# Performance work log

Measured on AMD Instinct MI355X. Metric: run time of the kernel, lower is better.

The kernel has to match this reference:

```python
import jax, jax.numpy as jnp
import numpy as np

B, C, H, W = 256, 768, 14, 14
S = 196  # sample_size
HID = 512
OUT = 2


def setup_inputs() -> dict:
    key = jax.random.key(0)
    ks = jax.random.split(key, 10)
    x = jax.random.normal(ks[0], (B, C, H, W), dtype=jnp.float32)
    pxs = jax.random.randint(ks[1], (B, S, 2), 0, H, dtype=jnp.int32)
    pys = jax.random.randint(ks[2], (B, S, 2), 0, H, dtype=jnp.int32)
    scale = 0.02
    W1 = jax.random.normal(ks[3], (2 * C, HID), dtype=jnp.float32) * scale
    b1 = jnp.zeros((HID,), dtype=jnp.float32)
    W2 = jax.random.normal(ks[4], (HID, HID), dtype=jnp.float32) * scale
    b2 = jnp.zeros((HID,), dtype=jnp.float32)
    W3 = jax.random.normal(ks[5], (HID, OUT), dtype=jnp.float32) * scale
    b3 = jnp.zeros((OUT,), dtype=jnp.float32)
    return {"x": x, "W1": W1, "b1": b1, "W2": W2, "b2": b2,
            "W3": W3, "b3": b3, "pxs": pxs, "pys": pys}


def _gather_pts(x_flat, pxy):
    # x_flat: [B, C, H*W]; pxy: [B, S, 2] -> [B, S, C]
    idx = pxy[:, :, 0] * W + pxy[:, :, 1]            # [B, S]
    g = jnp.take_along_axis(x_flat, idx[:, None, :].astype(jnp.int32), axis=2)  # [B, C, S]
    return g.transpose(0, 2, 1)                       # [B, S, C]


def reference(x, W1, b1, W2, b2, W3, b3, pxs, pys):
    x_flat = x.reshape(B, C, H * W)
    ptsx = _gather_pts(x_flat, pxs)                   # [B, S, C]
    ptsy = _gather_pts(x_flat, pys)                   # [B, S, C]
    feats = jnp.concatenate([ptsx, ptsy], axis=2)     # [B, S, 2C]
    h = jax.nn.relu(feats @ W1 + b1)
    h = jax.nn.relu(h @ W2 + b2)
    pred = h @ W3 + b3                                # [B, S, 2]
    predxy = pred.reshape(-1, OUT)                    # [B*S, 2]
    # use_abs=False, normalize=False: deltaxy = (pxs - pys) + (H - 1)
    deltaxy = (pxs - pys).astype(jnp.float32).reshape(-1, 2) + (H - 1)
    return predxy, deltaxy
```

## Files before the change

### kernel.cpp

```cpp
#include <hip/hip_runtime.h>
#include <hip/hip_bf16.h>

typedef __attribute__((ext_vector_type(4))) float f32x4;
typedef __attribute__((ext_vector_type(4))) int   int4v;
typedef __attribute__((ext_vector_type(8))) int   int8v;

__device__ __forceinline__ unsigned char f2fp8(float f) {
    unsigned char s = (__float_as_uint(f) >> 24) & 0x80;
    float a = fabsf(f);
    if (a >= 448.f) return s | 0x7E;
    if (a < 0.015625f) {
        int q = (int)(a * 512.0f + 0.5f);
        return s | (unsigned char)q;
    }
    unsigned int u = __float_as_uint(a);
    u += 0x0007FFFF + ((u >> 20) & 1);
    int e8 = (int)((u >> 23) & 0xFF) - 120;
    if (e8 >= 16) return s | 0x7E;
    return s | (unsigned char)((e8 << 3) | ((u >> 20) & 7));
}
__device__ __forceinline__ void gload_lds16(const void* g, void* l) {
    __builtin_amdgcn_global_load_lds((const __attribute__((address_space(1))) void*)g,
                                     (__attribute__((address_space(3))) void*)l, 16, 0, 0);
}

#define BATCH 256
#define CHAN  768
#define HW    196
#define SPS   196
#define HID   512
#define MROWS 50176
#define K1    1536
#define WSCL  64.0f
#define WINV  0.015625f
#define SC1   0x7F7F7F7F


__global__ void transpose_cast_fp8(const float* __restrict__ in, unsigned char* __restrict__ out,
                                   int K, int N) {
    int idx = blockIdx.x * 256 + threadIdx.x;
    if (idx >= K * N) return;
    int n = idx / K, k = idx - n * K;
    out[idx] = f2fp8(in[(size_t)k * N + n] * WSCL);
}

__global__ __launch_bounds__(256) void gather_feats(const float* __restrict__ x,
                                                    const int* __restrict__ pxs,
                                                    const int* __restrict__ pys,
                                                    unsigned char* __restrict__ feats,
                                                    float* __restrict__ out) {
    __shared__ float lds[64 * 197];
    int chunk = blockIdx.x;
    int b     = blockIdx.y;
    int c0 = chunk * 64;
    const float* xb = x + ((size_t)b * CHAN + c0) * HW;
    for (int t = threadIdx.x; t < 64 * HW; t += 256) {
        int j = t / HW, p = t - j * HW;
        lds[j * 197 + p] = xb[t];
    }
    if (chunk == 0) {
        for (int i = threadIdx.x; i < SPS * 2; i += 256) {
            int idx = b * SPS * 2 + i;
            out[MROWS * 2 + idx] = (float)(pxs[idx] - pys[idx]) + 13.0f;
        }
    }
    __syncthreads();
    int wid = threadIdx.x >> 6, lane = threadIdx.x & 63;
    int g = lane >> 4;
    int cq = (lane & 15) * 4;
    for (int sb = wid * 4; sb < SPS; sb += 16) {
        int s = sb + g;
        int base = (b * SPS + s) * 2;
        int ix = pxs[base] * 14 + pxs[base + 1];
        int iy = pys[base] * 14 + pys[base + 1];
        const float* lx = lds + cq * 197;
        unsigned int ux = 0, uy = 0;
        ux = __builtin_amdgcn_cvt_pk_fp8_f32(lx[ix],       lx[197 + ix], ux, false);
        ux = __builtin_amdgcn_cvt_pk_fp8_f32(lx[394 + ix], lx[591 + ix], ux, true);
        uy = __builtin_amdgcn_cvt_pk_fp8_f32(lx[iy],       lx[197 + iy], uy, false);
        uy = __builtin_amdgcn_cvt_pk_fp8_f32(lx[394 + iy], lx[591 + iy], uy, true);
        size_t ro = (size_t)(b * SPS + s) * K1;
        *(unsigned int*)(feats + ro + c0 + cq)        = ux;
        *(unsigned int*)(feats + ro + CHAN + c0 + cq) = uy;
    }
}

__global__ __launch_bounds__(512, 1) void mlp_fused(const unsigned char* __restrict__ feats,
                                                    const unsigned char* __restrict__ W1t,
                                                    const float* __restrict__ b1,
                                                    const unsigned char* __restrict__ W2t,
                                                    const float* __restrict__ b2,
                                                    const float* __restrict__ W3,
                                                    const float* __restrict__ b3,
                                                    float* __restrict__ out) {
    extern __shared__ char smem[];
    const int t = threadIdx.x;
    const int wid = t >> 6, lane = t & 63;
    const int wr = wid >> 2, wcn = wid & 3;
    const int lr = lane & 15, lk = lane >> 4;
    const int mBase = blockIdx.x * 128;
    f32x4 acc[4][8] = {};

    auto stage1 = [&](int buf, int kt) {
        char* Ab = smem + buf * 16384;
        char* Bb = smem + 32768 + buf * 65536;
        #pragma unroll
        for (int i = 0; i < 2; ++i) {
            int lin = i * 512 + t, row = lin >> 3, cs = (lin & 7) ^ (row & 7);
            gload_lds16(feats + (size_t)(mBase + row) * K1 + kt * 128 + cs * 16,
                        Ab + lin * 16);
        }
        #pragma unroll
        for (int i = 0; i < 8; ++i) {
            int lin = i * 512 + t, row = lin >> 3, cs = (lin & 7) ^ (row & 7);
            gload_lds16(W1t + (size_t)row * K1 + kt * 128 + cs * 16,
                        Bb + lin * 16);
        }
    };
    auto frag128 = [&](const char* rowp, int r) -> int8v {
        union { int4v h[2]; int8v v; } u;
        u.h[0] = *(const int4v*)(rowp + (((2 * lk + 0) ^ (r & 7)) * 16));
        u.h[1] = *(const int4v*)(rowp + (((2 * lk + 1) ^ (r & 7)) * 16));
        return u.v;
    };
    auto compute1 = [&](int buf) {
        const char* Ab = smem + buf * 16384;
        const char* Bb = smem + 32768 + buf * 65536;
        int8v af[4];
        #pragma unroll
        for (int m = 0; m < 4; ++m) {
            int r = wr * 64 + m * 16 + lr;
            af[m] = frag128(Ab + r * 128, r);
        }
        #pragma unroll
        for (int half = 0; half < 2; ++half) {
            int8v bf4[4];
            #pragma unroll
            for (int n = 0; n < 4; ++n) {
                int r = wcn * 128 + (half * 4 + n) * 16 + lr;
                bf4[n] = frag128(Bb + r * 128, r);
            }
            #pragma unroll
            for (int m = 0; m < 4; ++m)
                #pragma unroll
                for (int n = 0; n < 4; ++n)
                    acc[m][half * 4 + n] = __builtin_amdgcn_mfma_scale_f32_16x16x128_f8f6f4(
                        af[m], bf4[n], acc[m][half * 4 + n], 0, 0, 0, SC1, 0, SC1);
        }
    };

    stage1(0, 0);
    __syncthreads();
    int cur = 0;
    for (int kt = 0; kt < 12; ++kt) {
        if (kt + 1 < 12) stage1(cur ^ 1, kt + 1);
        compute1(cur);
        __syncthreads();
        cur ^= 1;
    }

    char* h1l = smem + 32768;
    char* B2b0 = smem;
    char* B2b1 = smem + 16384;
    #pragma unroll
    for (int n = 0; n < 8; ++n) {
        int c = wcn * 128 + n * 16 + lr;
        int c16 = wcn * 8 + n;
        float bv = b1[c];
        #pragma unroll
        for (int m = 0; m < 4; ++m) {
            int r0 = wr * 64 + m * 16 + lk * 4;
            float v0 = fmaxf(acc[m][n][0] * WINV + bv, 0.f);
            float v1 = fmaxf(acc[m][n][1] * WINV + bv, 0.f);
            float v2 = fmaxf(acc[m][n][2] * WINV + bv, 0.f);
            float v3 = fmaxf(acc[m][n][3] * WINV + bv, 0.f);
            unsigned int u = __builtin_amdgcn_cvt_pk_fp8_f32(v0, v1, 0u, false);
            u = __builtin_amdgcn_cvt_pk_fp8_f32(v2, v3, u, true);
            #pragma unroll
            for (int j = 0; j < 4; ++j) {
                int r = r0 + j;
                h1l[r * 512 + ((c16 ^ (r & 31)) * 16) + lr] =
                    (unsigned char)((u >> (8 * j)) & 0xff);
            }
        }
    }

    auto stageB2 = [&](char* dst, int p) {
        #pragma unroll
        for (int i = 0; i < 2; ++i) {
            int lin = i * 512 + t, row2 = lin >> 5, c = lin & 31;
            gload_lds16(W2t + (size_t)(p * 32 + row2) * 512 + ((c ^ row2) * 16),
                        dst + lin * 16);
        }
    };
    auto frag512 = [&](const char* base, int r, int kt2) -> int8v {
        int g = kt2 * 8 + lk * 2;
        union { int4v h[2]; int8v v; } u;
        u.h[0] = *(const int4v*)(base + r * 512 + (((g + 0) ^ (r & 31)) * 16));
        u.h[1] = *(const int4v*)(base + r * 512 + (((g + 1) ^ (r & 31)) * 16));
        return u.v;
    };

    float pp0[4] = {0.f, 0.f, 0.f, 0.f}, pp1[4] = {0.f, 0.f, 0.f, 0.f};
    stageB2(B2b0, 0);
    __syncthreads();
    for (int p = 0; p < 16; ++p) {
        char* curB = (p & 1) ? B2b1 : B2b0;
        char* nxtB = (p & 1) ? B2b0 : B2b1;
        if (p + 1 < 16) stageB2(nxtB, p + 1);
        f32x4 acc2[2] = {};
        #pragma unroll
        for (int kt2 = 0; kt2 < 4; ++kt2) {
            int8v a2 = frag512(h1l, wid * 16 + lr, kt2);
            #pragma unroll
            for (int n2 = 0; n2 < 2; ++n2) {
                int8v b2f = frag512(curB, n2 * 16 + lr, kt2);
                acc2[n2] = __builtin_amdgcn_mfma_scale_f32_16x16x128_f8f6f4(
                    a2, b2f, acc2[n2], 0, 0, 0, SC1, 0, SC1);
            }
        }
        #pragma unroll
        for (int n2 = 0; n2 < 2; ++n2) {
            int c2 = p * 32 + n2 * 16 + lr;
            float bv = b2[c2], w30 = W3[c2 * 2], w31 = W3[c2 * 2 + 1];
            #pragma unroll
            for (int j = 0; j < 4; ++j) {
                float v = fmaxf(acc2[n2][j] * WINV + bv, 0.f);
                pp0[j] += v * w30;
                pp1[j] += v * w31;
            }
        }
        __syncthreads();
    }

    float bb0 = b3[0], bb1 = b3[1];
    #pragma unroll
    for (int j = 0; j < 4; ++j) {
        float p0 = pp0[j], p1 = pp1[j];
        #pragma unroll
        for (int msk = 1; msk < 16; msk <<= 1) {
            p0 += __shfl_xor(p0, msk);
            p1 += __shfl_xor(p1, msk);
        }
        if (lr == 0) {
            int r = mBase + wid * 16 + lk * 4 + j;
            out[(size_t)r * 2 + 0] = p0 + bb0;
            out[(size_t)r * 2 + 1] = p1 + bb1;
        }
    }
}

extern "C" void kernel_launch(void* const* d_in, const int* in_sizes, int n_in,
                              void* d_out, int out_size, void* d_ws, size_t ws_size,
                              hipStream_t stream) {
    const float* x  = (const float*)d_in[0];
    const float* W1 = (const float*)d_in[1];
    const float* b1 = (const float*)d_in[2];
    const float* W2 = (const float*)d_in[3];
    const float* b2 = (const float*)d_in[4];
    const float* W3 = (const float*)d_in[5];
    const float* b3 = (const float*)d_in[6];
    const int*  pxs = (const int*)d_in[7];
    const int*  pys = (const int*)d_in[8];
    float* out = (float*)d_out;
    char* ws = (char*)d_ws;

    unsigned char* W1t   = (unsigned char*)(ws + 0);
    unsigned char* W2t   = (unsigned char*)(ws + 786432);
    unsigned char* feats = (unsigned char*)(ws + 1048576);

    hipFuncSetAttribute((const void*)mlp_fused,
                        hipFuncAttributeMaxDynamicSharedMemorySize, 163840);

    transpose_cast_fp8<<<(K1 * HID + 255) / 256, 256, 0, stream>>>(W1, W1t, K1, HID);
    transpose_cast_fp8<<<(HID * HID + 255) / 256, 256, 0, stream>>>(W2, W2t, HID, HID);
    gather_feats<<<dim3(12, BATCH), 256, 0, stream>>>(x, pxs, pys, feats, out);
    mlp_fused<<<MROWS / 128, 512, 163840, stream>>>(feats, W1t, b1, W2t, b2, W3, b3, out);
}
```

Measured before the change: 166.3 us.

## Double MLP block to 16 waves and keep W2 fragments in registers

The fused MLP kernel goes from 512 to 1024 threads per block. Each wave now owns a 64-column slice of layer 1 instead of 128, which halves the accumulator registers per thread. For layer 2, each wave loads its 32-column slice of W2 directly from global memory into registers and loops over all 128 rows of h1. This removes the double-buffered LDS staging of W2 and its per-step barriers. Partial layer-3 sums are then reduced across waves through an LDS buffer, which adds one barrier and a small reduction step, and register pressure per thread may limit how well the larger block schedules.

Result: slower. 271.0 us (+62.9%).

```diff
diff --git a/kernel.cpp b/kernel.cpp
--- a/kernel.cpp
+++ b/kernel.cpp
@@ -85,34 +85,33 @@
     }
 }
 
-__global__ __launch_bounds__(512, 1) void mlp_fused(const unsigned char* __restrict__ feats,
-                                                    const unsigned char* __restrict__ W1t,
-                                                    const float* __restrict__ b1,
-                                                    const unsigned char* __restrict__ W2t,
-                                                    const float* __restrict__ b2,
-                                                    const float* __restrict__ W3,
-                                                    const float* __restrict__ b3,
-                                                    float* __restrict__ out) {
+__global__ __launch_bounds__(1024) void mlp_fused(const unsigned char* __restrict__ feats,
+                                                  const unsigned char* __restrict__ W1t,
+                                                  const float* __restrict__ b1,
+                                                  const unsigned char* __restrict__ W2t,
+                                                  const float* __restrict__ b2,
+                                                  const float* __restrict__ W3,
+                                                  const float* __restrict__ b3,
+                                                  float* __restrict__ out) {
     extern __shared__ char smem[];
     const int t = threadIdx.x;
     const int wid = t >> 6, lane = t & 63;
-    const int wr = wid >> 2, wcn = wid & 3;
+    const int wr = wid >> 3, wcn = wid & 7;
     const int lr = lane & 15, lk = lane >> 4;
     const int mBase = blockIdx.x * 128;
-    f32x4 acc[4][8] = {};
+    f32x4 acc[4][4] = {};
 
     auto stage1 = [&](int buf, int kt) {
         char* Ab = smem + buf * 16384;
         char* Bb = smem + 32768 + buf * 65536;
-        #pragma unroll
-        for (int i = 0; i < 2; ++i) {
-            int lin = i * 512 + t, row = lin >> 3, cs = (lin & 7) ^ (row & 7);
+        {
+            int lin = t, row = lin >> 3, cs = (lin & 7) ^ (row & 7);
             gload_lds16(feats + (size_t)(mBase + row) * K1 + kt * 128 + cs * 16,
                         Ab + lin * 16);
         }
         #pragma unroll
-        for (int i = 0; i < 8; ++i) {
-            int lin = i * 512 + t, row = lin >> 3, cs = (lin & 7) ^ (row & 7);
+        for (int i = 0; i < 4; ++i) {
+            int lin = i * 1024 + t, row = lin >> 3, cs = (lin & 7) ^ (row & 7);
             gload_lds16(W1t + (size_t)row * K1 + kt * 128 + cs * 16,
                         Bb + lin * 16);
         }
@@ -133,19 +132,13 @@
             af[m] = frag128(Ab + r * 128, r);
         }
         #pragma unroll
-        for (int half = 0; half < 2; ++half) {
-            int8v bf4[4];
-            #pragma unroll
-            for (int n = 0; n < 4; ++n) {
-                int r = wcn * 128 + (half * 4 + n) * 16 + lr;
-                bf4[n] = frag128(Bb + r * 128, r);
-            }
+        for (int n = 0; n < 4; ++n) {
+            int r = wcn * 64 + n * 16 + lr;
+            int8v bf = frag128(Bb + r * 128, r);
             #pragma unroll
             for (int m = 0; m < 4; ++m)
-                #pragma unroll
-                for (int n = 0; n < 4; ++n)
-                    acc[m][half * 4 + n] = __builtin_amdgcn_mfma_scale_f32_16x16x128_f8f6f4(
-                        af[m], bf4[n], acc[m][half * 4 + n], 0, 0, 0, SC1, 0, SC1);
+                acc[m][n] = __builtin_amdgcn_mfma_scale_f32_16x16x128_f8f6f4(
+                    af[m], bf, acc[m][n], 0, 0, 0, SC1, 0, SC1);
         }
     };
 
@@ -159,13 +152,21 @@
         cur ^= 1;
     }
 
+    int8v b2f[2][4];
+    #pragma unroll
+    for (int n2 = 0; n2 < 2; ++n2) {
+        const unsigned char* rp = W2t + (size_t)(wid * 32 + n2 * 16 + lr) * 512;
+        #pragma unroll
+        for (int kt2 = 0; kt2 < 4; ++kt2)
+            b2f[n2][kt2] = *(const int8v*)(rp + kt2 * 128 + lk * 32);
+    }
+
     char* h1l = smem + 32768;
-    char* B2b0 = smem;
-    char* B2b1 = smem + 16384;
+    float* red = (float*)smem;
     #pragma unroll
-    for (int n = 0; n < 8; ++n) {
-        int c = wcn * 128 + n * 16 + lr;
-        int c16 = wcn * 8 + n;
+    for (int n = 0; n < 4; ++n) {
+        int c = wcn * 64 + n * 16 + lr;
+        int c16 = wcn * 4 + n;
         float bv = b1[c];
         #pragma unroll
         for (int m = 0; m < 4; ++m) {
@@ -184,69 +185,61 @@
             }
         }
     }
-
-    auto stageB2 = [&](char* dst, int p) {
-        #pragma unroll
-        for (int i = 0; i < 2; ++i) {
-            int lin = i * 512 + t, row2 = lin >> 5, c = lin & 31;
-            gload_lds16(W2t + (size_t)(p * 32 + row2) * 512 + ((c ^ row2) * 16),
-                        dst + lin * 16);
-        }
-    };
-    auto frag512 = [&](const char* base, int r, int kt2) -> int8v {
+    __syncthreads();
+
+    auto frag512 = [&](int r, int kt2) -> int8v {
         int g = kt2 * 8 + lk * 2;
         union { int4v h[2]; int8v v; } u;
-        u.h[0] = *(const int4v*)(base + r * 512 + (((g + 0) ^ (r & 31)) * 16));
-        u.h[1] = *(const int4v*)(base + r * 512 + (((g + 1) ^ (r & 31)) * 16));
+        u.h[0] = *(const int4v*)(h1l + r * 512 + (((g + 0) ^ (r & 31)) * 16));
+        u.h[1] = *(const int4v*)(h1l + r * 512 + (((g + 1) ^ (r & 31)) * 16));
         return u.v;
     };
-
-    float pp0[4] = {0.f, 0.f, 0.f, 0.f}, pp1[4] = {0.f, 0.f, 0.f, 0.f};
-    stageB2(B2b0, 0);
-    __syncthreads();
-    for (int p = 0; p < 16; ++p) {
-        char* curB = (p & 1) ? B2b1 : B2b0;
-        char* nxtB = (p & 1) ? B2b0 : B2b1;
-        if (p + 1 < 16) stageB2(nxtB, p + 1);
+    #pragma unroll
+    for (int s = 0; s < 8; ++s) {
         f32x4 acc2[2] = {};
         #pragma unroll
         for (int kt2 = 0; kt2 < 4; ++kt2) {
-            int8v a2 = frag512(h1l, wid * 16 + lr, kt2);
-            #pragma unroll
-            for (int n2 = 0; n2 < 2; ++n2) {
-                int8v b2f = frag512(curB, n2 * 16 + lr, kt2);
-                acc2[n2] = __builtin_amdgcn_mfma_scale_f32_16x16x128_f8f6f4(
-                    a2, b2f, acc2[n2], 0, 0, 0, SC1, 0, SC1);
-            }
-        }
+            int8v a2 = frag512(s * 16 + lr, kt2);
+            acc2[0] = __builtin_amdgcn_mfma_scale_f32_16x16x128_f8f6f4(
+                a2, b2f[0][kt2], acc2[0], 0, 0, 0, SC1, 0, SC1);
+            acc2[1] = __builtin_amdgcn_mfma_scale_f32_16x16x128_f8f6f4(
+                a2, b2f[1][kt2], acc2[1], 0, 0, 0, SC1, 0, SC1);
+        }
+        float p0[4] = {0.f, 0.f, 0.f, 0.f}, p1[4] = {0.f, 0.f, 0.f, 0.f};
         #pragma unroll
         for (int n2 = 0; n2 < 2; ++n2) {
-            int c2 = p * 32 + n2 * 16 + lr;
+            int c2 = wid * 32 + n2 * 16 + lr;
             float bv = b2[c2], w30 = W3[c2 * 2], w31 = W3[c2 * 2 + 1];
             #pragma unroll
             for (int j = 0; j < 4; ++j) {
                 float v = fmaxf(acc2[n2][j] * WINV + bv, 0.f);
-                pp0[j] += v * w30;
-                pp1[j] += v * w31;
-            }
-        }
-        __syncthreads();
-    }
-
-    float bb0 = b3[0], bb1 = b3[1];
-    #pragma unroll
-    for (int j = 0; j < 4; ++j) {
-        float p0 = pp0[j], p1 = pp1[j];
-        #pragma unroll
-        for (int msk = 1; msk < 16; msk <<= 1) {
-            p0 += __shfl_xor(p0, msk);
-            p1 += __shfl_xor(p1, msk);
-        }
-        if (lr == 0) {
-            int r = mBase + wid * 16 + lk * 4 + j;
-            out[(size_t)r * 2 + 0] = p0 + bb0;
-            out[(size_t)r * 2 + 1] = p1 + bb1;
-        }
+                p0[j] += v * w30;
+                p1[j] += v * w31;
+            }
+        }
+        #pragma unroll
+        for (int j = 0; j < 4; ++j) {
+            #pragma unroll
+            for (int msk = 1; msk < 16; msk <<= 1) {
+                p0[j] += __shfl_xor(p0[j], msk);
+                p1[j] += __shfl_xor(p1[j], msk);
+            }
+            if (lr == 0) {
+                int r = s * 16 + lk * 4 + j;
+                red[r * 33 + wid * 2 + 0] = p0[j];
+                red[r * 33 + wid * 2 + 1] = p1[j];
+            }
+        }
+    }
+    __syncthreads();
+
+    if (t < 256) {
+        int row = t >> 1, comp = t & 1;
+        float v = b3[comp];
+        #pragma unroll
+        for (int w = 0; w < 16; ++w)
+            v += red[row * 33 + w * 2 + comp];
+        out[(size_t)(mBase + row) * 2 + comp] = v;
     }
 }
 
@@ -275,5 +268,5 @@
     transpose_cast_fp8<<<(K1 * HID + 255) / 256, 256, 0, stream>>>(W1, W1t, K1, HID);
     transpose_cast_fp8<<<(HID * HID + 255) / 256, 256, 0, stream>>>(W2, W2t, HID, HID);
     gather_feats<<<dim3(12, BATCH), 256, 0, stream>>>(x, pxs, pys, feats, out);
-    mlp_fused<<<MROWS / 128, 512, 163840, stream>>>(feats, W1t, b1, W2t, b2, W3, b3, out);
-}
+    mlp_fused<<<MROWS / 128, 1024, 163840, stream>>>(feats, W1t, b1, W2t, b2, W3, b3, out);
+}
```

## Keep W2 fragments in registers and split layer-2 columns across waves

Applied to the files above, without the earlier changes.

Layer 2 used to stream W2 through LDS in 16 double-buffered passes, each wave handling 16 rows against every column. Now each wave loads its own 64 output columns of W2 directly into registers once and loops over all 128 rows of h1 from LDS. Per-wave partial sums for layer 3 are combined through a small LDS reduction buffer. This removes 16 barrier-synchronised staging steps, at the cost of a large register footprint (64 int registers for the B fragments) and an extra cross-wave reduction.

Measured after the change: 192.6 us. 15.8% more time.

```diff
diff --git a/kernel.cpp b/kernel.cpp
--- a/kernel.cpp
+++ b/kernel.cpp
@@ -160,8 +160,7 @@
     }
 
     char* h1l = smem + 32768;
-    char* B2b0 = smem;
-    char* B2b1 = smem + 16384;
+    float* red = (float*)smem;
     #pragma unroll
     for (int n = 0; n < 8; ++n) {
         int c = wcn * 128 + n * 16 + lr;
@@ -184,69 +183,76 @@
             }
         }
     }
-
-    auto stageB2 = [&](char* dst, int p) {
-        #pragma unroll
-        for (int i = 0; i < 2; ++i) {
-            int lin = i * 512 + t, row2 = lin >> 5, c = lin & 31;
-            gload_lds16(W2t + (size_t)(p * 32 + row2) * 512 + ((c ^ row2) * 16),
-                        dst + lin * 16);
-        }
-    };
-    auto frag512 = [&](const char* base, int r, int kt2) -> int8v {
+    __syncthreads();
+
+    int8v b2f[4][4];
+    #pragma unroll
+    for (int n2 = 0; n2 < 4; ++n2) {
+        const unsigned char* rp = W2t + (size_t)(wid * 64 + n2 * 16 + lr) * 512;
+        #pragma unroll
+        for (int kt2 = 0; kt2 < 4; ++kt2)
+            b2f[n2][kt2] = *(const int8v*)(rp + kt2 * 128 + lk * 32);
+    }
+    float bv2[4], w30[4], w31[4];
+    #pragma unroll
+    for (int n2 = 0; n2 < 4; ++n2) {
+        int c2 = wid * 64 + n2 * 16 + lr;
+        bv2[n2] = b2[c2];
+        w30[n2] = W3[c2 * 2];
+        w31[n2] = W3[c2 * 2 + 1];
+    }
+
+    auto frag512 = [&](int r, int kt2) -> int8v {
         int g = kt2 * 8 + lk * 2;
         union { int4v h[2]; int8v v; } u;
-        u.h[0] = *(const int4v*)(base + r * 512 + (((g + 0) ^ (r & 31)) * 16));
-        u.h[1] = *(const int4v*)(base + r * 512 + (((g + 1) ^ (r & 31)) * 16));
+        u.h[0] = *(const int4v*)(h1l + r * 512 + (((g + 0) ^ (r & 31)) * 16));
+        u.h[1] = *(const int4v*)(h1l + r * 512 + (((g + 1) ^ (r & 31)) * 16));
         return u.v;
     };
-
-    float pp0[4] = {0.f, 0.f, 0.f, 0.f}, pp1[4] = {0.f, 0.f, 0.f, 0.f};
-    stageB2(B2b0, 0);
-    __syncthreads();
-    for (int p = 0; p < 16; ++p) {
-        char* curB = (p & 1) ? B2b1 : B2b0;
-        char* nxtB = (p & 1) ? B2b0 : B2b1;
-        if (p + 1 < 16) stageB2(nxtB, p + 1);
-        f32x4 acc2[2] = {};
+    #pragma unroll
+    for (int s = 0; s < 8; ++s) {
+        f32x4 acc2[4] = {};
         #pragma unroll
         for (int kt2 = 0; kt2 < 4; ++kt2) {
-            int8v a2 = frag512(h1l, wid * 16 + lr, kt2);
-            #pragma unroll
-            for (int n2 = 0; n2 < 2; ++n2) {
-                int8v b2f = frag512(curB, n2 * 16 + lr, kt2);
+            int8v a2 = frag512(s * 16 + lr, kt2);
+            #pragma unroll
+            for (int n2 = 0; n2 < 4; ++n2)
                 acc2[n2] = __builtin_amdgcn_mfma_scale_f32_16x16x128_f8f6f4(
-                    a2, b2f, acc2[n2], 0, 0, 0, SC1, 0, SC1);
-            }
-        }
-        #pragma unroll
-        for (int n2 = 0; n2 < 2; ++n2) {
-            int c2 = p * 32 + n2 * 16 + lr;
-            float bv = b2[c2], w30 = W3[c2 * 2], w31 = W3[c2 * 2 + 1];
+                    a2, b2f[n2][kt2], acc2[n2], 0, 0, 0, SC1, 0, SC1);
+        }
+        float p0[4] = {0.f, 0.f, 0.f, 0.f}, p1[4] = {0.f, 0.f, 0.f, 0.f};
+        #pragma unroll
+        for (int n2 = 0; n2 < 4; ++n2) {
             #pragma unroll
             for (int j = 0; j < 4; ++j) {
-                float v = fmaxf(acc2[n2][j] * WINV + bv, 0.f);
-                pp0[j] += v * w30;
-                pp1[j] += v * w31;
-            }
-        }
-        __syncthreads();
-    }
-
-    float bb0 = b3[0], bb1 = b3[1];
-    #pragma unroll
-    for (int j = 0; j < 4; ++j) {
-        float p0 = pp0[j], p1 = pp1[j];
-        #pragma unroll
-        for (int msk = 1; msk < 16; msk <<= 1) {
-            p0 += __shfl_xor(p0, msk);
-            p1 += __shfl_xor(p1, msk);
-        }
-        if (lr == 0) {
-            int r = mBase + wid * 16 + lk * 4 + j;
-            out[(size_t)r * 2 + 0] = p0 + bb0;
-            out[(size_t)r * 2 + 1] = p1 + bb1;
-        }
+                float v = fmaxf(acc2[n2][j] * WINV + bv2[n2], 0.f);
+                p0[j] += v * w30[n2];
+                p1[j] += v * w31[n2];
+            }
+        }
+        #pragma unroll
+        for (int j = 0; j < 4; ++j) {
+            #pragma unroll
+            for (int msk = 1; msk < 16; msk <<= 1) {
+                p0[j] += __shfl_xor(p0[j], msk);
+                p1[j] += __shfl_xor(p1[j], msk);
+            }
+            if (lr == 0) {
+                int r = s * 16 + lk * 4 + j;
+                red[r * 17 + wid * 2 + 0] = p0[j];
+                red[r * 17 + wid * 2 + 1] = p1[j];
+            }
+        }
+    }
+    __syncthreads();
+
+    if (t < 256) {
+        int row = t >> 1, comp = t & 1;
+        float v = b3[comp];
+        #pragma unroll
+        for (int w = 0; w < 8; ++w)
+            v += red[row * 17 + w * 2 + comp];
+        out[(size_t)(mBase + row) * 2 + comp] = v;
     }
 }
 
```
